# Performance work log

Measured on AMD Instinct MI355X. Metric: run time of the kernel, lower is better.

Reference implementation:

```python
import jax, jax.numpy as jnp
import numpy as np

N_NODES = 100000
N_EDGES = 1600000
IN_CH = 128
OUT_CH = 128
N_REL = 64
N_BASES = 8


def setup_inputs() -> dict:
    key = jax.random.key(0)
    k = jax.random.split(key, 7)
    x = jax.random.normal(k[0], (N_NODES, IN_CH), dtype=jnp.float32)
    src = jax.random.randint(k[1], (N_EDGES,), 0, N_NODES, dtype=jnp.int32)
    rel = jax.random.randint(k[2], (N_EDGES,), 0, N_REL, dtype=jnp.int32)
    dst = jax.random.randint(k[3], (N_EDGES,), 0, N_NODES, dtype=jnp.int32)
    edge_triples = jnp.stack([src, rel, dst], axis=1)  # [E, 3] (src, rel, dst)
    # xavier-uniform-ish scales
    basis = jax.random.normal(k[4], (N_BASES, IN_CH, OUT_CH), dtype=jnp.float32) * (2.0 / (IN_CH + OUT_CH)) ** 0.5
    att = jax.random.normal(k[5], (N_REL, N_BASES), dtype=jnp.float32) * (2.0 / (N_REL + N_BASES)) ** 0.5
    root_w = jax.random.normal(k[6], (IN_CH, OUT_CH), dtype=jnp.float32) * (1.0 / IN_CH) ** 0.5
    root_b = jnp.zeros((OUT_CH,), dtype=jnp.float32)
    return {"x": x, "edge_triples": edge_triples, "num_nodes": N_NODES,
            "basis": basis, "att": att, "root_w": root_w, "root_b": root_b}


def reference(x, edge_triples, num_nodes, basis, att, root_w, root_b):
    src = edge_triples[:, 0]
    rel = edge_triples[:, 1]
    dst = edge_triples[:, 2]
    att_e = att[rel]  # [E, B]
    n_bases = basis.shape[0]
    e = src.shape[0]
    out_ch = basis.shape[2]
    # messages[e] = x[src[e]] @ (sum_b att[rel[e], b] * basis[b])
    # computed as sum_b att_e[:, b] * (x @ basis[b])[src] to avoid the huge
    # per-edge [E, in, out] weight gather the torch code materializes.
    msgs = jnp.zeros((e, out_ch), dtype=x.dtype)
    for b in range(n_bases):  # small fixed loop over bases
        yb = x @ basis[b]  # [N, out]
        msgs = msgs + att_e[:, b:b + 1] * yb[src]
    # degree normalization (mean aggregation over incoming edges)
    deg = jax.ops.segment_sum(jnp.ones((e,), dtype=x.dtype), dst, num_segments=num_nodes)
    deg_inv = jnp.where(deg > 0, 1.0 / deg, 0.0)
    msgs = msgs * deg_inv[dst][:, None]
    agg = jax.ops.segment_sum(msgs, dst, num_segments=num_nodes)  # [N, out]
    return agg + x @ root_w + root_b
```

## Files before the change

kernel.cpp:

```cpp
#include <hip/hip_runtime.h>

#define NCH 128
#define NREL 64
#define NBP 1024
#define ESB 4096
#define CAPF 3072
#define CAPH 2048
#define KTOT 1152
#define KST 36
#define ZROW 2304

typedef __attribute__((ext_vector_type(8))) short bf16x8;
typedef __attribute__((ext_vector_type(4))) float f32x4;

__device__ __forceinline__ unsigned short f2bf(float f) {
    unsigned u = __float_as_uint(f);
    return (unsigned short)((u + 0x7fffu + ((u >> 16) & 1u)) >> 16);
}
__device__ __forceinline__ unsigned pack2bf(float a, float b) {
    return (unsigned)f2bf(a) | ((unsigned)f2bf(b) << 16);
}

__global__ __launch_bounds__(256) void k_prep(const float* __restrict__ x,
                                              unsigned short* __restrict__ xsw,
                                              int N) {
    int idx = blockIdx.x * 256 + threadIdx.x;
    if (idx >= N * 16) return;
    int n = idx >> 4, l15 = idx & 15;
    const float* xr = x + (size_t)n * NCH + l15;
    bf16x8 p;
#pragma unroll
    for (int nt = 0; nt < 8; ++nt) p[nt] = (short)f2bf(xr[nt * 16]);
    *(bf16x8*)(xsw + (size_t)n * NCH + l15 * 8) = p;
}

__global__ __launch_bounds__(256) void k_buildB(const float* __restrict__ basis,
                                                const float* __restrict__ att,
                                                const float* __restrict__ rw,
                                                unsigned short* __restrict__ attB,
                                                unsigned short* __restrict__ basisP) {
    int idx = blockIdx.x * 256 + threadIdx.x;
    if (idx < 1040) {
        int rr = idx >> 4, b = idx & 15;
        attB[idx] = (rr < NREL && b < 8) ? f2bf(att[rr * 8 + b]) : (unsigned short)0;
    }
    if (idx >= 128 * KTOT) return;
    int j = idx & 7, lg = (idx >> 3) & 3, oc = (idx >> 5) & 127, kk = idx >> 12;
    int k = kk * 32 + lg * 8 + j;
    float v;
    if (k < 1024) {
        int b = k & 7, ch = k >> 3;
        v = basis[(size_t)b * NCH * NCH + (size_t)ch * NCH + oc];
    } else {
        int kp = k - 1024;
        int ic = ((kp & 7) << 4) | (kp >> 3);
        v = rw[(size_t)ic * NCH + oc];
    }
    basisP[idx] = f2bf(v);
}

__global__ __launch_bounds__(256) void k_count(const int* __restrict__ trip, int E, int NB,
                                               int* __restrict__ cntB) {
    __shared__ int hb[NBP];
    int t = threadIdx.x;
    for (int i = t; i < NB; i += 256) hb[i] = 0;
    __syncthreads();
    int base = blockIdx.x * ESB;
#pragma unroll
    for (int i = 0; i < ESB / 256; ++i) {
        int e = base + i * 256 + t;
        if (e < E) atomicAdd(&hb[trip[3 * e + 2] >> 7], 1);
    }
    __syncthreads();
    for (int i = t; i < NB; i += 256) cntB[(size_t)blockIdx.x * NB + i] = hb[i];
}

__global__ __launch_bounds__(1024) void k_scanB(int* __restrict__ cntB, int GB, int NB,
                                                int* __restrict__ bhist) {
    __shared__ int sc[1024];
    int t = threadIdx.x, b = blockIdx.x;
    int v = (t < GB) ? cntB[(size_t)t * NB + b] : 0;
    sc[t] = v;
    __syncthreads();
    for (int off = 1; off < 1024; off <<= 1) {
        int a = (t >= off) ? sc[t - off] : 0;
        __syncthreads();
        sc[t] += a;
        __syncthreads();
    }
    if (t < GB) cntB[(size_t)t * NB + b] = sc[t] - v;
    if (t == GB - 1) bhist[b] = sc[t];
}

__global__ __launch_bounds__(1024) void k_offsets(const int* __restrict__ bhist, int NB,
                                                  int* __restrict__ bucketoff) {
    __shared__ int sc[1024];
    int t = threadIdx.x;
    int d = (t < NB) ? bhist[t] : 0;
    sc[t] = d;
    __syncthreads();
    for (int off = 1; off < 1024; off <<= 1) {
        int a = (t >= off) ? sc[t - off] : 0;
        __syncthreads();
        sc[t] += a;
        __syncthreads();
    }
    if (t < NB) bucketoff[t] = sc[t] - d;
    if (t == NB - 1) bucketoff[NB] = sc[t];
}

__global__ __launch_bounds__(256) void k_scatter(const int* __restrict__ trip, int E, int NB,
                                                 const int* __restrict__ cntB,
                                                 const int* __restrict__ bucketoff,
                                                 unsigned* __restrict__ packed) {
    __shared__ int cb[NBP], lbase[NBP], delta[NBP];
    __shared__ int ssc[256];
    __shared__ unsigned lpk[ESB];
    __shared__ unsigned short lb[ESB];
    int t = threadIdx.x, blk = blockIdx.x;
    for (int i = t; i < NB; i += 256) cb[i] = 0;
    __syncthreads();
    int base = blk * ESB;
    int total = min(ESB, E - base);

    unsigned pk[ESB / 256];
    int rk[ESB / 256];
    unsigned short bk[ESB / 256];
#pragma unroll
    for (int i = 0; i < ESB / 256; ++i) {
        int e = base + i * 256 + t;
        pk[i] = 0; rk[i] = 0; bk[i] = 0;
        if (e < E) {
            int src = trip[3 * e], rel = trip[3 * e + 1], dst = trip[3 * e + 2];
            int bkt = dst >> 7;
            bk[i] = (unsigned short)bkt;
            pk[i] = ((unsigned)(dst & 127) << 23) | ((unsigned)rel << 17) | (unsigned)src;
            rk[i] = atomicAdd(&cb[bkt], 1);
        }
    }
    __syncthreads();
    int ch = (NB + 255) >> 8;
    int mysum = 0;
    for (int i = 0; i < ch; ++i) {
        int idx = t * ch + i;
        if (idx < NB) mysum += cb[idx];
    }
    ssc[t] = mysum;
    __syncthreads();
    for (int off = 1; off < 256; off <<= 1) {
        int a = (t >= off) ? ssc[t - off] : 0;
        __syncthreads();
        ssc[t] += a;
        __syncthreads();
    }
    int run = ssc[t] - mysum;
    for (int i = 0; i < ch; ++i) {
        int idx = t * ch + i;
        if (idx < NB) { lbase[idx] = run; run += cb[idx]; }
    }
    __syncthreads();
    for (int i = t; i < NB; i += 256)
        delta[i] = bucketoff[i] + cntB[(size_t)blk * NB + i] - lbase[i];
    __syncthreads();
#pragma unroll
    for (int i = 0; i < ESB / 256; ++i) {
        int e = base + i * 256 + t;
        if (e < E) {
            int j = lbase[bk[i]] + rk[i];
            lpk[j] = pk[i];
            lb[j] = bk[i];
        }
    }
    __syncthreads();
    for (int j = t; j < total; j += 256)
        packed[delta[lb[j]] + j] = lpk[j];
}

__global__ __launch_bounds__(256) void k_sortbkt(const unsigned* __restrict__ packed,
                                                 const int* __restrict__ bucketoff,
                                                 unsigned* __restrict__ sortedG,
                                                 int* __restrict__ dstoffG) {
    __shared__ int h[128], hs[128];
    int t = threadIdx.x, b = blockIdx.x;
    if (t < 128) h[t] = 0;
    __syncthreads();
    int s0 = bucketoff[b], s1 = bucketoff[b + 1];
    int cnt = min(s1 - s0, CAPF);

    unsigned pk[CAPF / 256];
    int rk[CAPF / 256];
#pragma unroll
    for (int i = 0; i < CAPF / 256; ++i) {
        int j = i * 256 + t;
        pk[i] = 0; rk[i] = 0;
        if (j < cnt) {
            unsigned p = packed[s0 + j];
            pk[i] = p;
            rk[i] = atomicAdd(&h[p >> 23], 1);
        }
    }
    __syncthreads();
    if (t < 128) hs[t] = h[t];
    __syncthreads();
    for (int off = 1; off < 128; off <<= 1) {
        int a = (t < 128 && t >= off) ? hs[t - off] : 0;
        __syncthreads();
        if (t < 128) hs[t] += a;
        __syncthreads();
    }
    if (t < 128) dstoffG[b * 129 + t] = hs[t] - h[t];
    if (t == 0) dstoffG[b * 129 + 128] = cnt;
#pragma unroll
    for (int i = 0; i < CAPF / 256; ++i) {
        int j = i * 256 + t;
        if (j < cnt) {
            int d = pk[i] >> 23;
            sortedG[s0 + hs[d] - h[d] + rk[i]] = pk[i];
        }
    }
}

__global__ __launch_bounds__(512, 4) void k_fused(const unsigned* __restrict__ x32,
                                                  const char* __restrict__ xswb,
                                                  const unsigned* __restrict__ sortedG,
                                                  const int* __restrict__ bucketoff,
                                                  const int* __restrict__ dstoffG,
                                                  const unsigned short* __restrict__ attBg,
                                                  const unsigned short* __restrict__ basisP,
                                                  const float* __restrict__ rb,
                                                  float* __restrict__ out, int N) {
    __shared__ bf16x8 ztV[16 * (ZROW / 16)];
    __shared__ unsigned sortedE[CAPH];
    __shared__ unsigned short attl[1056];
    __shared__ int doffsL[65];
    __shared__ int nextD;
    char* zt = (char*)ztV;

    int t = threadIdx.x;
    int bucket = blockIdx.x >> 1, half = blockIdx.x & 1;
    int w = t >> 6, lane = t & 63, lr = lane & 15, lg = lane >> 4;
    int l15 = lane & 15;
    int nb0 = bucket * 128 + half * 64;

    for (int i = t; i < 1040; i += 512) attl[i] = attBg[i];
    int rawIdx = bucket * 129 + half * 64;
    int rawBase = dstoffG[rawIdx];
    int cnt = min(dstoffG[rawIdx + 64] - rawBase, CAPH);
    if (t < 65) doffsL[t] = min(dstoffG[rawIdx + t] - rawBase, CAPH);
    if (t == 0) nextD = 0;
    int sG0 = bucketoff[bucket] + rawBase;
    for (int j = t; j < cnt; j += 512) {
        unsigned p = sortedG[sG0 + j];
        sortedE[j] = (((p >> 17) & 63u) << 26) | ((p & 0x1FFFFu) << 8);
    }
    __syncthreads();

    const char* xl = xswb + (l15 << 4);

    for (int r = 0; r < 4; ++r) {
        int rEnd = r * 16 + 16;

        for (;;) {
            int my = 0x7FFFFFFF;
            if (lane == 0) my = atomicAdd(&nextD, 1);
            my = __shfl(my, 0, 64);
            if (my >= rEnd) break;
            int d = my;
            int eBeg = doffsL[d], eEnd = doffsL[d + 1];
            int cnt_d = eEnd - eBeg;
            int n = nb0 + d;
            unsigned xv = (n < N) ? x32[(size_t)n * 64 + lane] : 0u;

            float inv = (cnt_d > 0) ? 1.f / (float)cnt_d : 0.f;
            int zr = d & 15, sw = zr & 7;
            char* zrow = zt + zr * ZROW;
            int last = eEnd - 1;

#pragma unroll 1
            for (int hp = 0; hp < 2; ++hp) {
                f32x4 acc[4];
#pragma unroll
                for (int q = 0; q < 4; ++q) acc[q] = (f32x4){0.f, 0.f, 0.f, 0.f};

                for (int c0 = eBeg; c0 < eEnd; c0 += 32) {
                    int kb = c0 + (lg << 3);
                    bf16x8 aF;
                    uint2 lo[8];
#pragma unroll
                    for (int j = 0; j < 8; ++j) {
                        int e = kb + j;
                        unsigned ew = sortedE[min(e, last)];
                        int arow = (e < eEnd) ? (int)(ew >> 26) : 64;
                        aF[j] = (short)attl[arow * 16 + l15];
                        lo[j] = *(const uint2*)(xl + (ew & 0x03FFFF00u) + hp * 8);
                    }
#pragma unroll
                    for (int q = 0; q < 4; ++q) {
                        unsigned sel = (q & 1) ? 0x03020706u : 0x01000504u;
                        int h = q >> 1;
                        unsigned bw[4];
                        bw[0] = __builtin_amdgcn_perm(((const unsigned*)&lo[0])[h],
                                                      ((const unsigned*)&lo[1])[h], sel);
                        bw[1] = __builtin_amdgcn_perm(((const unsigned*)&lo[2])[h],
                                                      ((const unsigned*)&lo[3])[h], sel);
                        bw[2] = __builtin_amdgcn_perm(((const unsigned*)&lo[4])[h],
                                                      ((const unsigned*)&lo[5])[h], sel);
                        bw[3] = __builtin_amdgcn_perm(((const unsigned*)&lo[6])[h],
                                                      ((const unsigned*)&lo[7])[h], sel);
                        acc[q] = __builtin_amdgcn_mfma_f32_16x16x32_bf16(
                            aF, *(const bf16x8*)&bw[0], acc[q], 0, 0, 0);
                    }
                }
                if (lane < 32) {
                    int b0 = (lane >> 4) << 2;
#pragma unroll
                    for (int q = 0; q < 4; ++q) {
                        int chn = (hp * 4 + q) * 16 + l15;
                        uint2 v;
                        v.x = pack2bf(acc[q][0] * inv, acc[q][1] * inv);
                        v.y = pack2bf(acc[q][2] * inv, acc[q][3] * inv);
                        *(uint2*)(zrow + ((chn ^ sw) << 4) + (b0 << 1)) = v;
                    }
                }
            }
            *(unsigned*)(zrow + (((128 + (lane >> 2)) ^ sw) << 4) + ((lane & 3) << 2)) = xv;
        }
        __syncthreads();

        f32x4 accM = {0.f, 0.f, 0.f, 0.f};
        int ocr = w * 16 + lr;
        int swm = lr & 7;
#pragma unroll 6
        for (int kk = 0; kk < KST; ++kk) {
            bf16x8 a = *(const bf16x8*)(zt + lr * ZROW + ((((kk << 2) + lg) ^ swm) << 4));
            bf16x8 b0 = *(const bf16x8*)(basisP + ((((size_t)kk * 128 + ocr) * 4 + lg) << 3));
            accM = __builtin_amdgcn_mfma_f32_16x16x32_bf16(b0, a, accM, 0, 0, 0);
        }

        int n = nb0 + r * 16 + lr;
        if (n < N) {
            int oc0 = w * 16 + lg * 4;
            f32x4 bias = *(const f32x4*)(rb + oc0);
            *(f32x4*)(out + (size_t)n * NCH + oc0) = accM + bias;
        }
        if (t == 0) nextD = rEnd;
        __syncthreads();
    }
}

extern "C" void kernel_launch(void* const* d_in, const int* in_sizes, int n_in,
                              void* d_out, int out_size, void* d_ws, size_t ws_size,
                              hipStream_t stream) {
    const float* x = (const float*)d_in[0];
    const int* trip = (const int*)d_in[1];
    const float* basis = (const float*)d_in[3];
    const float* att = (const float*)d_in[4];
    const float* rw = (const float*)d_in[5];
    const float* rb = (const float*)d_in[6];
    float* out = (float*)d_out;

    int N = in_sizes[0] / NCH;
    int E = in_sizes[1] / 3;
    int NB = (N + 127) >> 7;
    int GB = (E + ESB - 1) / ESB;

    char* ws = (char*)d_ws;
    size_t off = 0;
    auto alloc = [&](size_t bts) { size_t o = off; off = (off + bts + 255) & ~(size_t)255; return o; };
    size_t oXbf    = alloc((size_t)N * NCH * 2);
    size_t oBasisP = alloc((size_t)128 * KTOT * 2);
    size_t oAttB   = alloc(1056 * 2);
    size_t oCntB   = alloc((size_t)GB * NB * 4);
    size_t oBhist  = alloc((NBP + 1) * 4);
    size_t oBktoff = alloc((NBP + 1) * 4);
    size_t oPacked = alloc((size_t)E * 4);
    size_t oSorted = alloc((size_t)E * 4);
    size_t oDoff   = alloc((size_t)NB * 129 * 4);
    (void)off; (void)ws_size;

    unsigned short* x_sw = (unsigned short*)(ws + oXbf);
    unsigned short* basisP = (unsigned short*)(ws + oBasisP);
    unsigned short* attB = (unsigned short*)(ws + oAttB);
    int* cntB = (int*)(ws + oCntB);
    int* bhist = (int*)(ws + oBhist);
    int* bucketoff = (int*)(ws + oBktoff);
    unsigned* packed = (unsigned*)(ws + oPacked);
    unsigned* sortedG = (unsigned*)(ws + oSorted);
    int* dstoffG = (int*)(ws + oDoff);

    k_prep<<<(N * 16 + 255) / 256, 256, 0, stream>>>(x, x_sw, N);
    k_buildB<<<(128 * KTOT + 255) / 256, 256, 0, stream>>>(basis, att, rw, attB, basisP);
    k_count<<<GB, 256, 0, stream>>>(trip, E, NB, cntB);
    k_scanB<<<NB, 1024, 0, stream>>>(cntB, GB, NB, bhist);
    k_offsets<<<1, 1024, 0, stream>>>(bhist, NB, bucketoff);
    k_scatter<<<GB, 256, 0, stream>>>(trip, E, NB, cntB, bucketoff, packed);
    k_sortbkt<<<NB, 256, 0, stream>>>(packed, bucketoff, sortedG, dstoffG);
    k_fused<<<NB * 2, 512, 0, stream>>>((const unsigned*)x_sw, (const char*)x_sw, sortedG,
                                        bucketoff, dstoffG, attB, basisP, rb, out, N);
}
```

Baseline: 270.7 us.

## Pack two destination nodes per wave into one MFMA's 16 rows

Each wave now processes a pair of destination nodes instead of one. The attention table is expanded so the 16-row MFMA A operand holds 8 bases for the first node in rows 0-7 and 8 bases for the second node in rows 8-15, selected by a parity bit carried in each sorted edge word. Previously half the MFMA rows were zero padding. The change is meant to use MFMA throughput fully, halve per-edge-loop overhead, and let all lanes write results. The cost is a loop over the union of both nodes' edge ranges, plus a dependence on the low bit of dst being encoded in the packed edge word.

```diff
diff --git a/kernel.cpp b/kernel.cpp
--- a/kernel.cpp
+++ b/kernel.cpp
@@ -37,12 +37,13 @@
 __global__ __launch_bounds__(256) void k_buildB(const float* __restrict__ basis,
                                                 const float* __restrict__ att,
                                                 const float* __restrict__ rw,
-                                                unsigned short* __restrict__ attB,
+                                                unsigned short* __restrict__ attB2,
                                                 unsigned short* __restrict__ basisP) {
     int idx = blockIdx.x * 256 + threadIdx.x;
-    if (idx < 1040) {
-        int rr = idx >> 4, b = idx & 15;
-        attB[idx] = (rr < NREL && b < 8) ? f2bf(att[rr * 8 + b]) : (unsigned short)0;
+    if (idx < 2080) {
+        int rr = idx >> 5, p = (idx >> 4) & 1, m = idx & 15;
+        attB2[idx] = (rr < NREL && (m >> 3) == p) ? f2bf(att[rr * 8 + (m & 7)])
+                                                  : (unsigned short)0;
     }
     if (idx >= 128 * KTOT) return;
     int j = idx & 7, lg = (idx >> 3) & 3, oc = (idx >> 5) & 127, kk = idx >> 12;
@@ -231,7 +232,7 @@
                                                   float* __restrict__ out, int N) {
     __shared__ bf16x8 ztV[16 * (ZROW / 16)];
     __shared__ unsigned sortedE[CAPH];
-    __shared__ unsigned short attl[1056];
+    __shared__ unsigned short attl[2080];
     __shared__ int doffsL[65];
     __shared__ int nextD;
     char* zt = (char*)ztV;
@@ -242,7 +243,7 @@
     int l15 = lane & 15;
     int nb0 = bucket * 128 + half * 64;
 
-    for (int i = t; i < 1040; i += 512) attl[i] = attBg[i];
+    for (int i = t; i < 2080; i += 512) attl[i] = attBg[i];
     int rawIdx = bucket * 129 + half * 64;
     int rawBase = dstoffG[rawIdx];
     int cnt = min(dstoffG[rawIdx + 64] - rawBase, CAPH);
@@ -251,29 +252,35 @@
     int sG0 = bucketoff[bucket] + rawBase;
     for (int j = t; j < cnt; j += 512) {
         unsigned p = sortedG[sG0 + j];
-        sortedE[j] = (((p >> 17) & 63u) << 26) | ((p & 0x1FFFFu) << 8);
+        sortedE[j] = (((p >> 17) & 63u) << 26) | ((p & 0x1FFFFu) << 8) | ((p >> 23) & 1u);
     }
     __syncthreads();
 
     const char* xl = xswb + (l15 << 4);
 
     for (int r = 0; r < 4; ++r) {
-        int rEnd = r * 16 + 16;
+        int rEnd = r * 8 + 8;
 
         for (;;) {
             int my = 0x7FFFFFFF;
             if (lane == 0) my = atomicAdd(&nextD, 1);
             my = __shfl(my, 0, 64);
             if (my >= rEnd) break;
-            int d = my;
-            int eBeg = doffsL[d], eEnd = doffsL[d + 1];
-            int cnt_d = eEnd - eBeg;
-            int n = nb0 + d;
-            unsigned xv = (n < N) ? x32[(size_t)n * 64 + lane] : 0u;
-
-            float inv = (cnt_d > 0) ? 1.f / (float)cnt_d : 0.f;
-            int zr = d & 15, sw = zr & 7;
-            char* zrow = zt + zr * ZROW;
+            int d0 = my * 2, d1 = d0 + 1;
+            int eBeg = doffsL[d0], eMid = doffsL[d0 + 1], eEnd = doffsL[d0 + 2];
+            int cnt0 = eMid - eBeg, cnt1 = eEnd - eMid;
+            int n0 = nb0 + d0, n1 = nb0 + d1;
+            unsigned xv0 = (n0 < N) ? x32[(size_t)n0 * 64 + lane] : 0u;
+            unsigned xv1 = (n1 < N) ? x32[(size_t)n1 * 64 + lane] : 0u;
+
+            float inv0 = (cnt0 > 0) ? 1.f / (float)cnt0 : 0.f;
+            float inv1 = (cnt1 > 0) ? 1.f / (float)cnt1 : 0.f;
+            int pr = lg >> 1;
+            float invM = pr ? inv1 : inv0;
+            int dz = (pr ? d1 : d0) & 15;
+            char* zrowM = zt + dz * ZROW;
+            int swM = dz & 7;
+            int b0 = (lg & 1) << 2;
             int last = eEnd - 1;
 
 #pragma unroll 1
@@ -290,8 +297,9 @@
                     for (int j = 0; j < 8; ++j) {
                         int e = kb + j;
                         unsigned ew = sortedE[min(e, last)];
-                        int arow = (e < eEnd) ? (int)(ew >> 26) : 64;
-                        aF[j] = (short)attl[arow * 16 + l15];
+                        int arow = (e < eEnd) ? (int)(((ew >> 26) << 5) | ((ew & 1u) << 4))
+                                              : 2048;
+                        aF[j] = (short)attl[arow + l15];
                         lo[j] = *(const uint2*)(xl + (ew & 0x03FFFF00u) + hp * 8);
                     }
 #pragma unroll
@@ -311,19 +319,23 @@
                             aF, *(const bf16x8*)&bw[0], acc[q], 0, 0, 0);
                     }
                 }
-                if (lane < 32) {
-                    int b0 = (lane >> 4) << 2;
-#pragma unroll
-                    for (int q = 0; q < 4; ++q) {
-                        int chn = (hp * 4 + q) * 16 + l15;
-                        uint2 v;
-                        v.x = pack2bf(acc[q][0] * inv, acc[q][1] * inv);
-                        v.y = pack2bf(acc[q][2] * inv, acc[q][3] * inv);
-                        *(uint2*)(zrow + ((chn ^ sw) << 4) + (b0 << 1)) = v;
-                    }
+#pragma unroll
+                for (int q = 0; q < 4; ++q) {
+                    int chn = (hp * 4 + q) * 16 + l15;
+                    uint2 v;
+                    v.x = pack2bf(acc[q][0] * invM, acc[q][1] * invM);
+                    v.y = pack2bf(acc[q][2] * invM, acc[q][3] * invM);
+                    *(uint2*)(zrowM + ((chn ^ swM) << 4) + (b0 << 1)) = v;
                 }
             }
-            *(unsigned*)(zrow + (((128 + (lane >> 2)) ^ sw) << 4) + ((lane & 3) << 2)) = xv;
+            {
+                int z0 = d0 & 15, z1 = d1 & 15;
+                char* zr0 = zt + z0 * ZROW;
+                char* zr1 = zt + z1 * ZROW;
+                int u = 128 + (lane >> 2), sub = (lane & 3) << 2;
+                *(unsigned*)(zr0 + (((u) ^ (z0 & 7)) << 4) + sub) = xv0;
+                *(unsigned*)(zr1 + (((u) ^ (z1 & 7)) << 4) + sub) = xv1;
+            }
         }
         __syncthreads();
 
@@ -369,7 +381,7 @@
     auto alloc = [&](size_t bts) { size_t o = off; off = (off + bts + 255) & ~(size_t)255; return o; };
     size_t oXbf    = alloc((size_t)N * NCH * 2);
     size_t oBasisP = alloc((size_t)128 * KTOT * 2);
-    size_t oAttB   = alloc(1056 * 2);
+    size_t oAttB   = alloc(2080 * 2);
     size_t oCntB   = alloc((size_t)GB * NB * 4);
     size_t oBhist  = alloc((NBP + 1) * 4);
     size_t oBktoff = alloc((NBP + 1) * 4);
```

Measured after the change: 255.1 us. 5.8% less time.
